# Kernel optimization log

Measured on AMD Instinct MI355X. Metric: run time of the kernel, lower is better.

The kernel has to match this reference:

```python
import jax, jax.numpy as jnp
import numpy as np
from jax.scipy.special import logsumexp

HEAD = 12
EPS = 1.0


def _sinkhorn(dots):
    # dots: [b, h, n, n]. Faithful to the torch code: eps=1, max_iter=3,
    # update order u, v, u (the err<1e-6 early-break never triggers for
    # unconverged random-scale inputs, so we unroll the 3 iterations).
    C = -dots
    b, h, n, m = C.shape
    log_mu = -jnp.log(jnp.asarray(n, dtype=C.dtype))  # log(1/n)
    log_nu = -jnp.log(jnp.asarray(m, dtype=C.dtype))
    u = jnp.zeros((b, h, n), dtype=C.dtype)
    v = jnp.zeros((b, h, m), dtype=C.dtype)

    def M(u, v):
        # (-C + u_i + v_j) / eps
        return (-C + u[..., :, None] + v[..., None, :]) / EPS

    # i = 0: row update
    u = EPS * (log_mu - logsumexp(M(u, v), axis=-1)) + u
    # i = 1: column update (logsumexp over transpose == axis=-2)
    v = EPS * (log_nu - logsumexp(M(u, v), axis=-2)) + v
    # i = 2: row update
    u = EPS * (log_mu - logsumexp(M(u, v), axis=-1)) + u
    return jnp.exp(M(u, v))


def setup_inputs() -> dict:
    key = jax.random.key(0)
    ks = jax.random.split(key, 6)
    b, n, f = 8, 1024, 768
    x = jax.random.normal(ks[0], (b, n, f), dtype=jnp.float32)
    s = 1.0 / np.sqrt(f)
    Wq = jax.random.normal(ks[1], (f, f), dtype=jnp.float32) * s
    Wk = jax.random.normal(ks[2], (f, f), dtype=jnp.float32) * s
    Wv = jax.random.normal(ks[3], (f, f), dtype=jnp.float32) * s
    Wo = jax.random.normal(ks[4], (f, f), dtype=jnp.float32) * s
    bo = jax.random.normal(ks[5], (f,), dtype=jnp.float32) * 0.01
    return {"x": x, "Wq": Wq, "Wk": Wk, "Wv": Wv, "Wo": Wo, "bo": bo}


def reference(x, Wq, Wk, Wv, Wo, bo):
    b, n, f = x.shape
    h = HEAD
    d = f // h
    scale = d ** (-0.5)
    # nn.Linear: y = x @ W.T
    q = (x @ Wq.T).reshape(b, n, h, d).transpose(0, 2, 1, 3)  # [b,h,n,d]
    k = (x @ Wk.T).reshape(b, n, h, d).transpose(0, 2, 1, 3)
    v = (x @ Wv.T).reshape(b, n, h, d).transpose(0, 2, 1, 3)
    dots = jnp.einsum("bhid,bhjd->bhij", q, k) * scale  # [b,h,n,n]
    attn = _sinkhorn(dots)
    out = jnp.einsum("bhij,bhjd->bhid", attn, v)
    out = out.transpose(0, 2, 1, 3).reshape(b, n, f)
    return out @ Wo.T + bo
```

## Files before the change

### kernel.cpp

```cpp
#include <hip/hip_runtime.h>

#define DEV __device__ __forceinline__

typedef __attribute__((ext_vector_type(4))) float f32x4;
typedef __attribute__((ext_vector_type(8))) short bf16x8;

DEV short f2bf(float f) {
    union { float f; unsigned u; } v; v.f = f;
    unsigned r = (v.u + 0x7fffu + ((v.u >> 16) & 1u)) >> 16;
    return (short)r;
}

#ifndef __has_builtin
#define __has_builtin(x) 0
#endif
#if __has_builtin(__builtin_amdgcn_cvt_pk_bf16_f32)
DEV unsigned pkbf(float a, float b) {
    auto r = __builtin_amdgcn_cvt_pk_bf16_f32(a, b);
    union { __typeof__(r) v; unsigned u; } u; u.v = r; return u.u;
}
#else
DEV unsigned pkbf(float a, float b) {
    return (unsigned)(unsigned short)f2bf(a) | ((unsigned)(unsigned short)f2bf(b) << 16);
}
#endif

DEV void gl_lds16(const void* g, void* l) {
    __builtin_amdgcn_global_load_lds(
        (__attribute__((address_space(1))) void*)(g),
        (__attribute__((address_space(3))) void*)(l), 16, 0, 0);
}

template <int ITERS>
DEV void stage_tile(const short* g, int ldg, short* lds, int t) {
    const int w = t >> 6;
#pragma unroll
    for (int it = 0; it < ITERS; ++it) {
        int row = it * 32 + (t >> 3);
        int cx = (t & 7) ^ ((t >> 3) & 7);
        gl_lds16(g + row * ldg + cx * 8, (char*)lds + it * 4096 + (w << 10));
    }
}

DEV bf16x8 ldfrag(const short* lds, int r, int kc) {
    return *(const bf16x8*)(lds + r * 64 + ((kc ^ (r & 7)) << 3));
}

__global__ void cvt_all(const float* __restrict__ x,
                        const float* __restrict__ wq, const float* __restrict__ wk,
                        const float* __restrict__ wv, const float* __restrict__ wo,
                        short* __restrict__ xb,
                        short* __restrict__ wqb, short* __restrict__ wkb,
                        short* __restrict__ wvb, short* __restrict__ wob) {
    int b = blockIdx.x;
    const float* s; short* d; int i;
    if (b < 6144) {
        s = x; d = xb; i = b * 256 + threadIdx.x;
    } else {
        int r = b - 6144;
        int wi = r / 576, rem = r - wi * 576;
        s = (wi == 0) ? wq : (wi == 1) ? wk : (wi == 2) ? wv : wo;
        d = (wi == 0) ? wqb : (wi == 1) ? wkb : (wi == 2) ? wvb : wob;
        i = rem * 256 + threadIdx.x;
    }
    float4 v = ((const float4*)s)[i];
    short4 o;
    o.x = f2bf(v.x); o.y = f2bf(v.y); o.z = f2bf(v.z); o.w = f2bf(v.w);
    ((short4*)d)[i] = o;
}

#define TSTRIDE 136
__global__ __launch_bounds__(256) void proj_gemm(
    const short* __restrict__ xb,
    const short* __restrict__ wq, const short* __restrict__ wk, const short* __restrict__ wv,
    short* __restrict__ Qg, short* __restrict__ Kg, short* __restrict__ Vtg)
{
    __shared__ __align__(16) char smem[128 * TSTRIDE * 2];
    short* At = (short*)smem;
    short* Bt = (short*)(smem + 128 * 64 * 2);
    short* Ct = (short*)smem;
    const int t = threadIdx.x;
    const int z = blockIdx.z;
    const int row0 = blockIdx.x * 128, col0 = blockIdx.y * 128;
    const int lane = t & 63, w = t >> 6, quad = lane >> 4, c = lane & 15;
    const int wm = w >> 1, wn = w & 1;
    const short* W = (z == 0) ? wq : (z == 1) ? wk : wv;

    f32x4 acc[4][4];
#pragma unroll
    for (int i = 0; i < 4; ++i)
#pragma unroll
        for (int j = 0; j < 4; ++j) acc[i][j] = (f32x4){0.f, 0.f, 0.f, 0.f};

    for (int k0 = 0; k0 < 768; k0 += 64) {
        __syncthreads();
        stage_tile<4>(xb + (size_t)row0 * 768 + k0, 768, At, t);
        stage_tile<4>(W + (size_t)col0 * 768 + k0, 768, Bt, t);
        __syncthreads();
#pragma unroll
        for (int ks = 0; ks < 2; ++ks) {
            bf16x8 af[4], bfr[4];
#pragma unroll
            for (int fm = 0; fm < 4; ++fm) af[fm] = ldfrag(At, wm * 64 + fm * 16 + c, ks * 4 + quad);
#pragma unroll
            for (int fn = 0; fn < 4; ++fn) bfr[fn] = ldfrag(Bt, wn * 64 + fn * 16 + c, ks * 4 + quad);
#pragma unroll
            for (int fm = 0; fm < 4; ++fm)
#pragma unroll
                for (int fn = 0; fn < 4; ++fn)
                    acc[fm][fn] = __builtin_amdgcn_mfma_f32_16x16x32_bf16(af[fm], bfr[fn], acc[fm][fn], 0, 0, 0);
        }
    }

    __syncthreads();
    if (z == 2) {
#pragma unroll
        for (int fm = 0; fm < 4; ++fm)
#pragma unroll
            for (int fn = 0; fn < 4; ++fn) {
                int ddl = wn * 64 + fn * 16 + c;
                int rrl0 = wm * 64 + fm * 16 + quad * 4;
                short4 v4;
                v4.x = f2bf(acc[fm][fn][0]); v4.y = f2bf(acc[fm][fn][1]);
                v4.z = f2bf(acc[fm][fn][2]); v4.w = f2bf(acc[fm][fn][3]);
                *(short4*)(Ct + ddl * TSTRIDE + rrl0) = v4;
            }
    } else {
        const float sc = (z == 0) ? 0.125f * 1.4426950408889634f : 1.0f;
#pragma unroll
        for (int fm = 0; fm < 4; ++fm)
#pragma unroll
            for (int fn = 0; fn < 4; ++fn) {
                int rrl0 = wm * 64 + fm * 16 + quad * 4;
                int ddl = wn * 64 + fn * 16 + c;
#pragma unroll
                for (int reg = 0; reg < 4; ++reg)
                    Ct[(rrl0 + reg) * TSTRIDE + ddl] = f2bf(acc[fm][fn][reg] * sc);
            }
    }
    __syncthreads();

    const int bb = row0 >> 10;
#pragma unroll
    for (int it = 0; it < 8; ++it) {
        int row = it * 16 + (t >> 4);
        int ck = t & 15;
        bf16x8 v = *(const bf16x8*)(Ct + row * TSTRIDE + ck * 8);
        if (z == 2) {
            int gdd = col0 + row;
            int head = bb * 12 + (gdd >> 6);
            *(bf16x8*)(Vtg + ((size_t)head * 64 + (gdd & 63)) * 1024 + (row0 & 1023) + ck * 8) = v;
        } else {
            int rr = (row0 & 1023) + row;
            int gc = col0 + ck * 8;
            int head = bb * 12 + (gc >> 6);
            short* dst = (z == 0) ? Qg : Kg;
            *(bf16x8*)(dst + ((size_t)head * 1024 + rr) * 64 + (gc & 63)) = v;
        }
    }
}

__global__ __launch_bounds__(256) void lse_pass(
    const short* __restrict__ Aall, const short* __restrict__ Ball,
    const float* __restrict__ bias, float* __restrict__ outv,
    float bias_sign, float out_sign)
{
    __shared__ __align__(16) short At[128 * 64];
    __shared__ __align__(16) short Bt[128 * 64];
    __shared__ __align__(16) float biasl[1024];
    const int t = threadIdx.x;
    const int head = blockIdx.x % 96;
    const int r0 = (blockIdx.x / 96) * 128;
    const int lane = t & 63, w = t >> 6, quad = lane >> 4, c = lane & 15;
    const short* A = Aall + (size_t)head * 65536;
    const short* B = Ball + (size_t)head * 65536;

    stage_tile<4>(A + r0 * 64, 64, At, t);
    if (bias) {
        float4 v = ((const float4*)(bias + (size_t)head * 1024))[t];
        v.x *= bias_sign; v.y *= bias_sign; v.z *= bias_sign; v.w *= bias_sign;
        ((float4*)biasl)[t] = v;
    } else ((float4*)biasl)[t] = make_float4(0.f, 0.f, 0.f, 0.f);

    float lsum[2] = {0.f, 0.f};

    for (int j0 = 0; j0 < 1024; j0 += 128) {
        __syncthreads();
        stage_tile<4>(B + j0 * 64, 64, Bt, t);
        __syncthreads();
        f32x4 sacc[8][2];
#pragma unroll
        for (int fm = 0; fm < 8; ++fm)
#pragma unroll
            for (int fn = 0; fn < 2; ++fn) sacc[fm][fn] = (f32x4){0.f, 0.f, 0.f, 0.f};
#pragma unroll
        for (int ks = 0; ks < 2; ++ks) {
            bf16x8 af[8], bfr[2];
#pragma unroll
            for (int fm = 0; fm < 8; ++fm) af[fm] = ldfrag(Bt, fm * 16 + c, ks * 4 + quad);
#pragma unroll
            for (int fn = 0; fn < 2; ++fn) bfr[fn] = ldfrag(At, w * 32 + fn * 16 + c, ks * 4 + quad);
#pragma unroll
            for (int fm = 0; fm < 8; ++fm)
#pragma unroll
                for (int fn = 0; fn < 2; ++fn)
                    sacc[fm][fn] = __builtin_amdgcn_mfma_f32_16x16x32_bf16(af[fm], bfr[fn], sacc[fm][fn], 0, 0, 0);
        }
#pragma unroll
        for (int fm = 0; fm < 8; ++fm) {
            float4 b4 = *(const float4*)(biasl + j0 + fm * 16 + quad * 4);
#pragma unroll
            for (int fn = 0; fn < 2; ++fn) {
                float p0 = __builtin_amdgcn_exp2f(sacc[fm][fn][0] + b4.x);
                float p1 = __builtin_amdgcn_exp2f(sacc[fm][fn][1] + b4.y);
                float p2 = __builtin_amdgcn_exp2f(sacc[fm][fn][2] + b4.z);
                float p3 = __builtin_amdgcn_exp2f(sacc[fm][fn][3] + b4.w);
                lsum[fn] += (p0 + p1) + (p2 + p3);
            }
        }
    }

#pragma unroll
    for (int fn = 0; fn < 2; ++fn) {
        float s = lsum[fn];
        s += __shfl_xor(s, 16); s += __shfl_xor(s, 32);
        lsum[fn] = s;
    }
    if (quad == 0 && w < 4) {
#pragma unroll
        for (int fn = 0; fn < 2; ++fn)
            outv[(size_t)head * 1024 + r0 + w * 32 + fn * 16 + c] =
                out_sign * __builtin_amdgcn_logf(lsum[fn]);
    }
}

__global__ __launch_bounds__(256) void flash_pass(
    const short* __restrict__ Qall, const short* __restrict__ Kall,
    const short* __restrict__ Vtall, const float* __restrict__ v1,
    short* __restrict__ ctx)
{
    __shared__ __align__(16) short Qt[128 * 64];
    __shared__ __align__(16) short Kt[64 * 64];
    __shared__ __align__(16) short Vtl[64 * 64];
    __shared__ __align__(16) short Pl[4][32 * 72];
    __shared__ __align__(16) float v1l[1024];
    const int t = threadIdx.x;
    const int head = blockIdx.x % 96;
    const int r0 = (blockIdx.x / 96) * 128;
    const int lane = t & 63, w = t >> 6, quad = lane >> 4, c = lane & 15;
    const short* Q = Qall + (size_t)head * 65536;
    const short* K = Kall + (size_t)head * 65536;
    const short* Vt = Vtall + (size_t)head * 65536;

    stage_tile<4>(Q + r0 * 64, 64, Qt, t);
    ((float4*)v1l)[t] = ((const float4*)(v1 + (size_t)head * 1024))[t];

    float lsum[2] = {0.f, 0.f};
    f32x4 oacc[2][4];
#pragma unroll
    for (int fm = 0; fm < 2; ++fm)
#pragma unroll
        for (int fn = 0; fn < 4; ++fn) oacc[fm][fn] = (f32x4){0.f, 0.f, 0.f, 0.f};
    short* myP = Pl[w];

    for (int j0 = 0; j0 < 1024; j0 += 64) {
        __syncthreads();
        stage_tile<2>(K + j0 * 64, 64, Kt, t);
        stage_tile<2>(Vt + j0, 1024, Vtl, t);
        __syncthreads();
        f32x4 sacc[4][2];
#pragma unroll
        for (int fm = 0; fm < 4; ++fm)
#pragma unroll
            for (int fn = 0; fn < 2; ++fn) sacc[fm][fn] = (f32x4){0.f, 0.f, 0.f, 0.f};
#pragma unroll
        for (int ks = 0; ks < 2; ++ks) {
            bf16x8 af[4], bfr[2];
#pragma unroll
            for (int fm = 0; fm < 4; ++fm) af[fm] = ldfrag(Kt, fm * 16 + c, ks * 4 + quad);
#pragma unroll
            for (int fn = 0; fn < 2; ++fn) bfr[fn] = ldfrag(Qt, w * 32 + fn * 16 + c, ks * 4 + quad);
#pragma unroll
            for (int fm = 0; fm < 4; ++fm)
#pragma unroll
                for (int fn = 0; fn < 2; ++fn)
                    sacc[fm][fn] = __builtin_amdgcn_mfma_f32_16x16x32_bf16(af[fm], bfr[fn], sacc[fm][fn], 0, 0, 0);
        }
#pragma unroll
        for (int fm = 0; fm < 4; ++fm) {
            float4 b4 = *(const float4*)(v1l + j0 + fm * 16 + quad * 4);
#pragma unroll
            for (int fn = 0; fn < 2; ++fn) {
                float p0 = __builtin_amdgcn_exp2f(sacc[fm][fn][0] + b4.x);
                float p1 = __builtin_amdgcn_exp2f(sacc[fm][fn][1] + b4.y);
                float p2 = __builtin_amdgcn_exp2f(sacc[fm][fn][2] + b4.z);
                float p3 = __builtin_amdgcn_exp2f(sacc[fm][fn][3] + b4.w);
                lsum[fn] += (p0 + p1) + (p2 + p3);
                uint2 pk; pk.x = pkbf(p0, p1); pk.y = pkbf(p2, p3);
                *(uint2*)(myP + (fn * 16 + c) * 72 + fm * 16 + quad * 4) = pk;
            }
        }
        asm volatile("s_waitcnt lgkmcnt(0)" ::: "memory");
#pragma unroll
        for (int ks2 = 0; ks2 < 2; ++ks2) {
            bf16x8 paf[2], vbf[4];
#pragma unroll
            for (int fm = 0; fm < 2; ++fm)
                paf[fm] = *(const bf16x8*)(myP + (fm * 16 + c) * 72 + ks2 * 32 + quad * 8);
#pragma unroll
            for (int fn = 0; fn < 4; ++fn) vbf[fn] = ldfrag(Vtl, fn * 16 + c, ks2 * 4 + quad);
#pragma unroll
            for (int fm = 0; fm < 2; ++fm)
#pragma unroll
                for (int fn = 0; fn < 4; ++fn)
                    oacc[fm][fn] = __builtin_amdgcn_mfma_f32_16x16x32_bf16(paf[fm], vbf[fn], oacc[fm][fn], 0, 0, 0);
        }
    }

#pragma unroll
    for (int fn = 0; fn < 2; ++fn) {
        float s = lsum[fn];
        s += __shfl_xor(s, 16); s += __shfl_xor(s, 32);
        lsum[fn] = s;
    }
    const int bb = head / 12, hh = head % 12;
#pragma unroll
    for (int fm = 0; fm < 2; ++fm)
#pragma unroll
        for (int reg = 0; reg < 4; ++reg) {
            float nrm = __builtin_amdgcn_rcpf(1024.f * __shfl(lsum[fm], quad * 4 + reg, 64));
            int rr = r0 + w * 32 + fm * 16 + quad * 4 + reg;
#pragma unroll
            for (int fn = 0; fn < 4; ++fn)
                ctx[((size_t)(bb * 1024 + rr)) * 768 + hh * 64 + fn * 16 + c] =
                    f2bf(oacc[fm][fn][reg] * nrm);
        }
}

__global__ __launch_bounds__(256) void out_gemm(
    const short* __restrict__ ctxb, const short* __restrict__ wo,
    const float* __restrict__ bo, float* __restrict__ out)
{
    __shared__ __align__(16) short At[128 * 64];
    __shared__ __align__(16) short Bt[128 * 64];
    const int t = threadIdx.x;
    const int row0 = blockIdx.x * 128, col0 = blockIdx.y * 128;
    const int lane = t & 63, w = t >> 6, quad = lane >> 4, c = lane & 15;
    const int wm = w >> 1, wn = w & 1;

    f32x4 acc[4][4];
#pragma unroll
    for (int i = 0; i < 4; ++i)
#pragma unroll
        for (int j = 0; j < 4; ++j) acc[i][j] = (f32x4){0.f, 0.f, 0.f, 0.f};

    for (int k0 = 0; k0 < 768; k0 += 64) {
        __syncthreads();
        stage_tile<4>(ctxb + (size_t)row0 * 768 + k0, 768, At, t);
        stage_tile<4>(wo + (size_t)col0 * 768 + k0, 768, Bt, t);
        __syncthreads();
#pragma unroll
        for (int ks = 0; ks < 2; ++ks) {
            bf16x8 af[4], bfr[4];
#pragma unroll
            for (int fm = 0; fm < 4; ++fm) af[fm] = ldfrag(At, wm * 64 + fm * 16 + c, ks * 4 + quad);
#pragma unroll
            for (int fn = 0; fn < 4; ++fn) bfr[fn] = ldfrag(Bt, wn * 64 + fn * 16 + c, ks * 4 + quad);
#pragma unroll
            for (int fm = 0; fm < 4; ++fm)
#pragma unroll
                for (int fn = 0; fn < 4; ++fn)
                    acc[fm][fn] = __builtin_amdgcn_mfma_f32_16x16x32_bf16(af[fm], bfr[fn], acc[fm][fn], 0, 0, 0);
        }
    }
#pragma unroll
    for (int fm = 0; fm < 4; ++fm)
#pragma unroll
        for (int fn = 0; fn < 4; ++fn) {
            int gr0 = row0 + wm * 64 + fm * 16 + quad * 4;
            int gc = col0 + wn * 64 + fn * 16 + c;
            float b = bo[gc];
#pragma unroll
            for (int reg = 0; reg < 4; ++reg)
                out[(size_t)(gr0 + reg) * 768 + gc] = acc[fm][fn][reg] + b;
        }
}

extern "C" void kernel_launch(void* const* d_in, const int* in_sizes, int n_in,
                              void* d_out, int out_size, void* d_ws, size_t ws_size,
                              hipStream_t stream) {
    const float* x  = (const float*)d_in[0];
    const float* Wq = (const float*)d_in[1];
    const float* Wk = (const float*)d_in[2];
    const float* Wv = (const float*)d_in[3];
    const float* Wo = (const float*)d_in[4];
    const float* bo = (const float*)d_in[5];
    float* out = (float*)d_out;

    char* p = (char*)d_ws;
    short* xb  = (short*)p; p += (size_t)8192 * 768 * 2;
    short* wqb = (short*)p; p += (size_t)768 * 768 * 2;
    short* wkb = (short*)p; p += (size_t)768 * 768 * 2;
    short* wvb = (short*)p; p += (size_t)768 * 768 * 2;
    short* wob = (short*)p; p += (size_t)768 * 768 * 2;
    short* Qg  = (short*)p; p += (size_t)96 * 1024 * 64 * 2;
    short* Kg  = (short*)p; p += (size_t)96 * 1024 * 64 * 2;
    short* Vtg = (short*)p; p += (size_t)96 * 1024 * 64 * 2;
    float* r1  = (float*)p; p += (size_t)96 * 1024 * 4;
    float* v1  = (float*)p; p += (size_t)96 * 1024 * 4;
    short* ctx = (short*)p; p += (size_t)8192 * 768 * 2;

    cvt_all<<<6144 + 4 * 576, 256, 0, stream>>>(x, Wq, Wk, Wv, Wo, xb, wqb, wkb, wvb, wob);

    proj_gemm<<<dim3(64, 6, 3), 256, 0, stream>>>(xb, wqb, wkb, wvb, Qg, Kg, Vtg);

    lse_pass<<<768, 256, 0, stream>>>(Qg, Kg, nullptr, r1, 0.f, 1.f);
    lse_pass<<<768, 256, 0, stream>>>(Kg, Qg, r1, v1, -1.f, -1.f);

    flash_pass<<<768, 256, 0, stream>>>(Qg, Kg, Vtg, v1, ctx);

    out_gemm<<<dim3(64, 6), 256, 0, stream>>>(ctx, wob, bo, out);
}
```

Measured before the change: 258.0 us.

## Keep P in registers for PV MFMA by computing transposed output

The flash pass no longer writes the exponentiated score tile P to LDS and reads it back. The PV product is computed transposed (V^T as the A operand, P taken straight from the S accumulator layout as the B operand), so each lane's packed bf16 values feed the MFMA directly. V fragments are assembled from two 4-element LDS reads, which relies on the K-index permutation matching on both operands. The epilogue writes 4 contiguous bf16 per lane and drops the row-sum shuffle. Launch bounds now request 4 blocks per CU, trading register budget for occupancy.

```diff
diff --git a/kernel.cpp b/kernel.cpp
--- a/kernel.cpp
+++ b/kernel.cpp
@@ -4,6 +4,7 @@
 
 typedef __attribute__((ext_vector_type(4))) float f32x4;
 typedef __attribute__((ext_vector_type(8))) short bf16x8;
+typedef __attribute__((ext_vector_type(4))) short bf16x4;
 
 DEV short f2bf(float f) {
     union { float f; unsigned u; } v; v.f = f;
@@ -44,6 +45,11 @@
 
 DEV bf16x8 ldfrag(const short* lds, int r, int kc) {
     return *(const bf16x8*)(lds + r * 64 + ((kc ^ (r & 7)) << 3));
+}
+
+DEV bf16x4 ldv4(const short* lds, int r, int o) {
+    int chunk = o >> 3, sub = o & 7;
+    return *(const bf16x4*)(lds + r * 64 + ((chunk ^ (r & 7)) << 3) + sub);
 }
 
 __global__ void cvt_all(const float* __restrict__ x,
@@ -234,7 +240,7 @@
     }
 }
 
-__global__ __launch_bounds__(256) void flash_pass(
+__global__ __launch_bounds__(256, 4) void flash_pass(
     const short* __restrict__ Qall, const short* __restrict__ Kall,
     const short* __restrict__ Vtall, const float* __restrict__ v1,
     short* __restrict__ ctx)
@@ -242,7 +248,6 @@
     __shared__ __align__(16) short Qt[128 * 64];
     __shared__ __align__(16) short Kt[64 * 64];
     __shared__ __align__(16) short Vtl[64 * 64];
-    __shared__ __align__(16) short Pl[4][32 * 72];
     __shared__ __align__(16) float v1l[1024];
     const int t = threadIdx.x;
     const int head = blockIdx.x % 96;
@@ -256,12 +261,11 @@
     ((float4*)v1l)[t] = ((const float4*)(v1 + (size_t)head * 1024))[t];
 
     float lsum[2] = {0.f, 0.f};
-    f32x4 oacc[2][4];
-#pragma unroll
-    for (int fm = 0; fm < 2; ++fm)
-#pragma unroll
-        for (int fn = 0; fn < 4; ++fn) oacc[fm][fn] = (f32x4){0.f, 0.f, 0.f, 0.f};
-    short* myP = Pl[w];
+    f32x4 oacc[4][2];
+#pragma unroll
+    for (int md = 0; md < 4; ++md)
+#pragma unroll
+        for (int ni = 0; ni < 2; ++ni) oacc[md][ni] = (f32x4){0.f, 0.f, 0.f, 0.f};
 
     for (int j0 = 0; j0 < 1024; j0 += 64) {
         __syncthreads();
@@ -286,6 +290,7 @@
                 for (int fn = 0; fn < 2; ++fn)
                     sacc[fm][fn] = __builtin_amdgcn_mfma_f32_16x16x32_bf16(af[fm], bfr[fn], sacc[fm][fn], 0, 0, 0);
         }
+        unsigned pk[4][2][2];
 #pragma unroll
         for (int fm = 0; fm < 4; ++fm) {
             float4 b4 = *(const float4*)(v1l + j0 + fm * 16 + quad * 4);
@@ -296,24 +301,31 @@
                 float p2 = __builtin_amdgcn_exp2f(sacc[fm][fn][2] + b4.z);
                 float p3 = __builtin_amdgcn_exp2f(sacc[fm][fn][3] + b4.w);
                 lsum[fn] += (p0 + p1) + (p2 + p3);
-                uint2 pk; pk.x = pkbf(p0, p1); pk.y = pkbf(p2, p3);
-                *(uint2*)(myP + (fn * 16 + c) * 72 + fm * 16 + quad * 4) = pk;
-            }
-        }
-        asm volatile("s_waitcnt lgkmcnt(0)" ::: "memory");
-#pragma unroll
-        for (int ks2 = 0; ks2 < 2; ++ks2) {
-            bf16x8 paf[2], vbf[4];
-#pragma unroll
-            for (int fm = 0; fm < 2; ++fm)
-                paf[fm] = *(const bf16x8*)(myP + (fm * 16 + c) * 72 + ks2 * 32 + quad * 8);
-#pragma unroll
-            for (int fn = 0; fn < 4; ++fn) vbf[fn] = ldfrag(Vtl, fn * 16 + c, ks2 * 4 + quad);
-#pragma unroll
-            for (int fm = 0; fm < 2; ++fm)
-#pragma unroll
-                for (int fn = 0; fn < 4; ++fn)
-                    oacc[fm][fn] = __builtin_amdgcn_mfma_f32_16x16x32_bf16(paf[fm], vbf[fn], oacc[fm][fn], 0, 0, 0);
+                pk[fm][fn][0] = pkbf(p0, p1);
+                pk[fm][fn][1] = pkbf(p2, p3);
+            }
+        }
+#pragma unroll
+        for (int ks = 0; ks < 2; ++ks) {
+            bf16x8 vaf[4];
+#pragma unroll
+            for (int md = 0; md < 4; ++md) {
+                union { bf16x8 v8; bf16x4 h[2]; } u;
+                u.h[0] = ldv4(Vtl, md * 16 + c, ks * 32 + quad * 4);
+                u.h[1] = ldv4(Vtl, md * 16 + c, ks * 32 + 16 + quad * 4);
+                vaf[md] = u.v8;
+            }
+#pragma unroll
+            for (int ni = 0; ni < 2; ++ni) {
+                union { bf16x8 v8; unsigned u4[4]; } b;
+                b.u4[0] = pk[2 * ks + 0][ni][0];
+                b.u4[1] = pk[2 * ks + 0][ni][1];
+                b.u4[2] = pk[2 * ks + 1][ni][0];
+                b.u4[3] = pk[2 * ks + 1][ni][1];
+#pragma unroll
+                for (int md = 0; md < 4; ++md)
+                    oacc[md][ni] = __builtin_amdgcn_mfma_f32_16x16x32_bf16(vaf[md], b.v8, oacc[md][ni], 0, 0, 0);
+            }
         }
     }
 
@@ -325,16 +337,19 @@
     }
     const int bb = head / 12, hh = head % 12;
 #pragma unroll
-    for (int fm = 0; fm < 2; ++fm)
-#pragma unroll
-        for (int reg = 0; reg < 4; ++reg) {
-            float nrm = __builtin_amdgcn_rcpf(1024.f * __shfl(lsum[fm], quad * 4 + reg, 64));
-            int rr = r0 + w * 32 + fm * 16 + quad * 4 + reg;
-#pragma unroll
-            for (int fn = 0; fn < 4; ++fn)
-                ctx[((size_t)(bb * 1024 + rr)) * 768 + hh * 64 + fn * 16 + c] =
-                    f2bf(oacc[fm][fn][reg] * nrm);
-        }
+    for (int ni = 0; ni < 2; ++ni) {
+        float nrm = __builtin_amdgcn_rcpf(1024.f * lsum[ni]);
+        int rr = r0 + w * 32 + ni * 16 + c;
+#pragma unroll
+        for (int md = 0; md < 4; ++md) {
+            short4 v4;
+            v4.x = f2bf(oacc[md][ni][0] * nrm);
+            v4.y = f2bf(oacc[md][ni][1] * nrm);
+            v4.z = f2bf(oacc[md][ni][2] * nrm);
+            v4.w = f2bf(oacc[md][ni][3] * nrm);
+            *(short4*)(ctx + ((size_t)(bb * 1024 + rr)) * 768 + hh * 64 + md * 16 + quad * 4) = v4;
+        }
+    }
 }
 
 __global__ __launch_bounds__(256) void out_gemm(
```

Result: faster. 244.9 us (-5.1%).
